# Kernel optimization log

Measured on AMD Instinct MI355X. Metric: run time of the kernel, lower is better.

The kernel has to match this reference:

```python
import jax, jax.numpy as jnp
import numpy as np

K = 5  # neighbors per node


def build_knn_adjacency(x, k=K):
    # x: (B, N, D) -> adj: (B, N, N)
    B, N, D = x.shape
    x_norm = x / jnp.clip(jnp.linalg.norm(x, axis=-1, keepdims=True), 1e-12)
    sim = jnp.einsum('bnd,bmd->bnm', x_norm, x_norm)  # (B, N, N)
    eye = jnp.eye(N, dtype=bool)
    sim = jnp.where(eye[None], jnp.asarray(-1.0, sim.dtype), sim)
    _, knn_idx = jax.lax.top_k(sim, k)  # (B, N, k)
    b_ix = jnp.arange(B)[:, None, None]
    i_ix = jnp.arange(N)[None, :, None]
    adj = jnp.zeros((B, N, N), dtype=x.dtype).at[b_ix, i_ix, knn_idx].set(1.0)
    adj = adj + jnp.eye(N, dtype=x.dtype)[None]
    return adj


def gcn_layer(x, adj, W, b):
    # deg-normalized aggregation then linear (torch Linear: x @ W.T + b)
    deg = adj.sum(axis=-1, keepdims=True)
    adj_norm = adj / jnp.clip(deg, 1.0)
    out = jnp.einsum('bnm,bmd->bnd', adj_norm, x)
    return out @ W.T + b


def setup_inputs() -> dict:
    key = jax.random.key(0)
    k1, k2, k3, k4, k5 = jax.random.split(key, 5)
    B, N, D, H = 32, 1024, 128, 128
    scale = 1.0 / np.sqrt(D)
    return {
        'x': jax.random.normal(k1, (B, N, D), dtype=jnp.float32),
        'W1': jax.random.normal(k2, (H, D), dtype=jnp.float32) * scale,
        'b1': jax.random.normal(k3, (H,), dtype=jnp.float32) * 0.01,
        'W2': jax.random.normal(k4, (H, H), dtype=jnp.float32) * scale,
        'b2': jax.random.normal(k5, (H,), dtype=jnp.float32) * 0.01,
    }


def reference(x, W1, b1, W2, b2):
    adj = build_knn_adjacency(x, k=K)
    h = x + jax.nn.relu(gcn_layer(x, adj, W1, b1))
    h = h + jax.nn.relu(gcn_layer(h, adj, W2, b2))
    return h  # pool='none' -> (B, N, hidden_dim)
```

## Files before the change

kernel.cpp:

```cpp
#include <hip/hip_runtime.h>
#include <float.h>
#include <math.h>

#define BB 32
#define NN 1024
#define DD 128
#define KK 5

typedef __attribute__((ext_vector_type(8))) short bf16x8;
typedef __attribute__((ext_vector_type(4))) float f32x4;

__device__ __forceinline__ unsigned short f2bf(float f) {
    unsigned int u = __float_as_uint(f);
    return (unsigned short)((u + 0x7FFFu + ((u >> 16) & 1u)) >> 16);
}
__device__ __forceinline__ float bf2f(unsigned short h) {
    return __uint_as_float(((unsigned int)h) << 16);
}

__global__ __launch_bounds__(256) void k_norm(const float* __restrict__ x,
                                              unsigned short* __restrict__ ph,
                                              unsigned short* __restrict__ pm,
                                              unsigned short* __restrict__ pl) {
    int row  = blockIdx.x * 4 + (threadIdx.x >> 6);
    int lane = threadIdx.x & 63;
    float2 v = *reinterpret_cast<const float2*>(x + (size_t)row * DD + lane * 2);
    float ss = v.x * v.x + v.y * v.y;
#pragma unroll
    for (int o = 32; o >= 1; o >>= 1) ss += __shfl_xor(ss, o);
    float inv = 1.0f / fmaxf(sqrtf(ss), 1e-12f);
    float y0 = v.x * inv, y1 = v.y * inv;

    unsigned short h0 = f2bf(y0);             float r0 = y0 - bf2f(h0);
    unsigned short m0 = f2bf(r0);             float s0 = r0 - bf2f(m0);
    unsigned short l0 = f2bf(s0);
    unsigned short h1 = f2bf(y1);             float r1 = y1 - bf2f(h1);
    unsigned short m1 = f2bf(r1);             float s1 = r1 - bf2f(m1);
    unsigned short l1 = f2bf(s1);

    size_t o = (size_t)row * DD + lane * 2;
    *reinterpret_cast<unsigned int*>(ph + o) = (unsigned int)h0 | ((unsigned int)h1 << 16);
    *reinterpret_cast<unsigned int*>(pm + o) = (unsigned int)m0 | ((unsigned int)m1 << 16);
    *reinterpret_cast<unsigned int*>(pl + o) = (unsigned int)l0 | ((unsigned int)l1 << 16);
}

__device__ __forceinline__ void stage_plane(const unsigned short* __restrict__ g,
                                            unsigned short (*s)[40], int tid,
                                            size_t rowbase, int c) {
#pragma unroll
    for (int hh = 0; hh < 2; ++hh) {
        int u = tid + (hh << 8);
        int row = u >> 2, q = u & 3;
        const float4 v = *reinterpret_cast<const float4*>(
            g + (rowbase + row) * DD + (c << 5) + (q << 3));
        *reinterpret_cast<float4*>(&s[row][q << 3]) = v;
    }
}

__global__ __launch_bounds__(256, 2) void k_sim(const unsigned short* __restrict__ ph,
                                                const unsigned short* __restrict__ pm,
                                                const unsigned short* __restrict__ pl,
                                                float* __restrict__ sim, int b0) {
    int t  = blockIdx.x;
    int bl = t / 36;
    int p  = t - bl * 36;
    int ti = 0;
    while (p >= 8 - ti) { p -= 8 - ti; ++ti; }
    int tj = ti + p;
    int R  = ti << 7, Cc = tj << 7;

    __shared__ unsigned short Ah[128][40], Am[128][40], Al[128][40];
    __shared__ unsigned short Bh[128][40], Bm[128][40], Bl[128][40];

    int tid  = threadIdx.x;
    int wv   = tid >> 6;
    int lane = tid & 63;
    int wr = (wv >> 1) << 6;
    int wc = (wv & 1) << 6;

    size_t base  = (size_t)(b0 + bl) * NN;
    size_t rbA = base + R, rbB = base + Cc;

    f32x4 acc[4][4];
#pragma unroll
    for (int i = 0; i < 4; ++i)
#pragma unroll
        for (int j = 0; j < 4; ++j) acc[i][j] = (f32x4){0.f, 0.f, 0.f, 0.f};

    int kk = (lane >> 4) << 3;
    int fr = lane & 15;

    for (int c = 0; c < 4; ++c) {
        if (c) __syncthreads();
        stage_plane(ph, Ah, tid, rbA, c);
        stage_plane(pm, Am, tid, rbA, c);
        stage_plane(pl, Al, tid, rbA, c);
        stage_plane(ph, Bh, tid, rbB, c);
        stage_plane(pm, Bm, tid, rbB, c);
        stage_plane(pl, Bl, tid, rbB, c);
        __syncthreads();

        bf16x8 bh[4], bm[4], blo[4];
#pragma unroll
        for (int cp = 0; cp < 4; ++cp) {
            int rb = wc + cp * 16 + fr;
            bh[cp]  = *reinterpret_cast<const bf16x8*>(&Bh[rb][kk]);
            bm[cp]  = *reinterpret_cast<const bf16x8*>(&Bm[rb][kk]);
            blo[cp] = *reinterpret_cast<const bf16x8*>(&Bl[rb][kk]);
        }
#pragma unroll
        for (int rp = 0; rp < 4; ++rp) {
            int ra = wr + rp * 16 + fr;
            bf16x8 ah = *reinterpret_cast<const bf16x8*>(&Ah[ra][kk]);
            bf16x8 am = *reinterpret_cast<const bf16x8*>(&Am[ra][kk]);
            bf16x8 al = *reinterpret_cast<const bf16x8*>(&Al[ra][kk]);
#pragma unroll
            for (int cp = 0; cp < 4; ++cp) {
                f32x4 cacc = acc[rp][cp];
                cacc = __builtin_amdgcn_mfma_f32_16x16x32_bf16(ah, bh[cp],  cacc, 0, 0, 0);
                cacc = __builtin_amdgcn_mfma_f32_16x16x32_bf16(ah, bm[cp],  cacc, 0, 0, 0);
                cacc = __builtin_amdgcn_mfma_f32_16x16x32_bf16(am, bh[cp],  cacc, 0, 0, 0);
                cacc = __builtin_amdgcn_mfma_f32_16x16x32_bf16(ah, blo[cp], cacc, 0, 0, 0);
                cacc = __builtin_amdgcn_mfma_f32_16x16x32_bf16(al, bh[cp],  cacc, 0, 0, 0);
                cacc = __builtin_amdgcn_mfma_f32_16x16x32_bf16(am, bm[cp],  cacc, 0, 0, 0);
                acc[rp][cp] = cacc;
            }
        }
    }

    float* Cb = sim + (size_t)bl * NN * NN;
    int crow = R + wr + ((lane >> 4) << 2);
    int ccol = Cc + wc + fr;
#pragma unroll
    for (int rp = 0; rp < 4; ++rp)
#pragma unroll
        for (int reg = 0; reg < 4; ++reg) {
            size_t rowo = (size_t)(crow + rp * 16 + reg) * NN + ccol;
#pragma unroll
            for (int cp = 0; cp < 4; ++cp)
                Cb[rowo + cp * 16] = acc[rp][cp][reg];
        }
    if (ti != tj) {
#pragma unroll
        for (int cp = 0; cp < 4; ++cp) {
            size_t mr = (size_t)(Cc + wc + cp * 16 + fr) * NN + (R + wr + ((lane >> 4) << 2));
#pragma unroll
            for (int rp = 0; rp < 4; ++rp)
                *reinterpret_cast<float4*>(&Cb[mr + rp * 16]) =
                    make_float4(acc[rp][cp][0], acc[rp][cp][1], acc[rp][cp][2], acc[rp][cp][3]);
        }
    }
}

__global__ __launch_bounds__(256) void k_topk(const float* __restrict__ sim,
                                              int* __restrict__ idx, int b0) {
    int lrow = blockIdx.x * 4 + (threadIdx.x >> 6);
    int lane = threadIdx.x & 63;
    const float* sr = sim + (size_t)lrow * NN;
    int i = lrow & (NN - 1);

    float v[16];
#pragma unroll
    for (int q = 0; q < 4; ++q) {
        float4 f = *reinterpret_cast<const float4*>(sr + lane * 16 + q * 4);
        v[q * 4 + 0] = f.x; v[q * 4 + 1] = f.y; v[q * 4 + 2] = f.z; v[q * 4 + 3] = f.w;
    }
    if ((i >> 4) == lane) {
        int s = i & 15;
#pragma unroll
        for (int j = 0; j < 16; ++j) if (j == s) v[j] = -FLT_MAX;
    }
    int* op = idx + ((size_t)b0 * NN + lrow) * KK;
#pragma unroll
    for (int t = 0; t < KK; ++t) {
        float bv = v[0]; int bj = 0;
#pragma unroll
        for (int j = 1; j < 16; ++j) if (v[j] > bv) { bv = v[j]; bj = j; }
        int bm = (lane << 4) + bj;
#pragma unroll
        for (int o = 1; o < 64; o <<= 1) {
            float ov = __shfl_xor(bv, o);
            int   om = __shfl_xor(bm, o);
            if (ov > bv || (ov == bv && om < bm)) { bv = ov; bm = om; }
        }
        if ((bm >> 4) == lane) {
            int s = bm & 15;
#pragma unroll
            for (int j = 0; j < 16; ++j) if (j == s) v[j] = -FLT_MAX;
        }
        if (lane == 0) op[t] = bm;
    }
}

#define SW(c) ((c) + 4 * ((c) >> 5))
#define LDW 140

__global__ __launch_bounds__(256, 3) void k_gcn(const float* __restrict__ h,
                                                const int* __restrict__ idx,
                                                const float* __restrict__ W,
                                                const float* __restrict__ bias,
                                                const float* __restrict__ res,
                                                float* __restrict__ out) {
    int rt = blockIdx.x << 6;
    __shared__ float As[64][68];
    __shared__ float Bs[64][LDW];
    int tid = threadIdx.x;
    int tr  = (tid >> 4) << 2;
    int tc  = (tid & 15) << 3;
    int stc = SW(tc);

    float acc[4][8];
#pragma unroll
    for (int i = 0; i < 4; ++i)
#pragma unroll
        for (int j = 0; j < 8; ++j) acc[i][j] = 0.f;

#pragma unroll
    for (int kc = 0; kc < 2; ++kc) {
        if (kc) __syncthreads();
        {
            int kv = tid & 15, r0 = tid >> 4;
            int colf = (kc << 6) + (kv << 2);
#pragma unroll
            for (int p = 0; p < 4; ++p) {
                int lrow = r0 + (p << 4);
                int grow = rt + lrow;
                const int* ip = idx + (size_t)grow * KK;
                const float* hb = h + (((size_t)grow >> 10) << 10) * DD;
                float4 v = *reinterpret_cast<const float4*>(h + (size_t)grow * DD + colf);
#pragma unroll
                for (int t = 0; t < KK; ++t) {
                    const float4 u = *reinterpret_cast<const float4*>(hb + (size_t)ip[t] * DD + colf);
                    v.x += u.x; v.y += u.y; v.z += u.z; v.w += u.w;
                }
                const float c = 1.0f / 6.0f;
                int k = kv << 2;
                As[k + 0][lrow] = v.x * c; As[k + 1][lrow] = v.y * c;
                As[k + 2][lrow] = v.z * c; As[k + 3][lrow] = v.w * c;
            }
        }
        {
            int kv = tid & 15, r0 = tid >> 4;
            const float* g = W + kc * 64;
#pragma unroll
            for (int p = 0; p < 8; ++p) {
                int r = r0 + (p << 4);
                const float4 v = *reinterpret_cast<const float4*>(g + (size_t)r * DD + (kv << 2));
                int k = kv << 2, row = SW(r);
                Bs[k + 0][row] = v.x; Bs[k + 1][row] = v.y;
                Bs[k + 2][row] = v.z; Bs[k + 3][row] = v.w;
            }
        }
        __syncthreads();
#pragma unroll 4
        for (int k = 0; k < 64; ++k) {
            const float4 a  = *reinterpret_cast<const float4*>(&As[k][tr]);
            const float4 b0 = *reinterpret_cast<const float4*>(&Bs[k][stc]);
            const float4 b1 = *reinterpret_cast<const float4*>(&Bs[k][stc + 4]);
            const float av[4] = {a.x, a.y, a.z, a.w};
            const float bw[8] = {b0.x, b0.y, b0.z, b0.w, b1.x, b1.y, b1.z, b1.w};
#pragma unroll
            for (int ii = 0; ii < 4; ++ii)
#pragma unroll
                for (int jj = 0; jj < 8; ++jj)
                    acc[ii][jj] = fmaf(av[ii], bw[jj], acc[ii][jj]);
        }
    }
    const float4 bz0 = *reinterpret_cast<const float4*>(bias + tc);
    const float4 bz1 = *reinterpret_cast<const float4*>(bias + tc + 4);
    const float bb[8] = {bz0.x, bz0.y, bz0.z, bz0.w, bz1.x, bz1.y, bz1.z, bz1.w};
#pragma unroll
    for (int i = 0; i < 4; ++i) {
        size_t ro = (size_t)(rt + tr + i) * DD + tc;
        const float4 r0 = *reinterpret_cast<const float4*>(res + ro);
        const float4 r1 = *reinterpret_cast<const float4*>(res + ro + 4);
        float4 o0, o1;
        o0.x = r0.x + fmaxf(acc[i][0] + bb[0], 0.f);
        o0.y = r0.y + fmaxf(acc[i][1] + bb[1], 0.f);
        o0.z = r0.z + fmaxf(acc[i][2] + bb[2], 0.f);
        o0.w = r0.w + fmaxf(acc[i][3] + bb[3], 0.f);
        o1.x = r1.x + fmaxf(acc[i][4] + bb[4], 0.f);
        o1.y = r1.y + fmaxf(acc[i][5] + bb[5], 0.f);
        o1.z = r1.z + fmaxf(acc[i][6] + bb[6], 0.f);
        o1.w = r1.w + fmaxf(acc[i][7] + bb[7], 0.f);
        *reinterpret_cast<float4*>(out + ro)     = o0;
        *reinterpret_cast<float4*>(out + ro + 4) = o1;
    }
}

extern "C" void kernel_launch(void* const* d_in, const int* in_sizes, int n_in,
                              void* d_out, int out_size, void* d_ws, size_t ws_size,
                              hipStream_t stream) {
    const float* x  = (const float*)d_in[0];
    const float* W1 = (const float*)d_in[1];
    const float* b1 = (const float*)d_in[2];
    const float* W2 = (const float*)d_in[3];
    const float* b2 = (const float*)d_in[4];
    float* out = (float*)d_out;

    char* ws = (char*)d_ws;
    size_t pl_b  = (size_t)BB * NN * DD * 2;
    size_t h1_b  = (size_t)BB * NN * DD * 4;
    size_t idx_b = (size_t)BB * NN * KK * 4;
    unsigned short* ph = (unsigned short*)ws;  ws += pl_b;
    unsigned short* pm = (unsigned short*)ws;  ws += pl_b;
    unsigned short* pl = (unsigned short*)ws;  ws += pl_b;
    float* h1  = (float*)ws;                   ws += h1_b;
    int*   idx = (int*)ws;                     ws += idx_b;
    float* sim = (float*)ws;
    size_t fixed = 3 * pl_b + h1_b + idx_b;
    size_t sim_avail = (ws_size > fixed) ? (ws_size - fixed) : 0;
    int SB = (int)(sim_avail / ((size_t)NN * NN * 4));
    if (SB > BB) SB = BB;
    if (SB < 1) SB = 1;

    k_norm<<<BB * NN / 4, 256, 0, stream>>>(x, ph, pm, pl);
    for (int b0 = 0; b0 < BB; b0 += SB) {
        int sb = (SB < BB - b0) ? SB : (BB - b0);
        k_sim<<<sb * 36, 256, 0, stream>>>(ph, pm, pl, sim, b0);
        k_topk<<<sb * NN / 4, 256, 0, stream>>>(sim, idx, b0);
    }
    k_gcn<<<BB * NN / 64, 256, 0, stream>>>(x,  idx, W1, b1, x,  h1);
    k_gcn<<<BB * NN / 64, 256, 0, stream>>>(h1, idx, W2, b2, h1, out);
}
```

Measured before the change: 172.1 us.

## Fuse top-k selection into similarity GEMM epilogue with partial candidate merge

Instead of writing the full N×N similarity matrix to global memory and running a separate top-k pass, each sim tile now computes per-row top-5 candidates in registers and shared memory, then writes them to a compact candidate buffer. A new merge kernel reduces the 16 partial candidate lists per row into the final 5 indices. This removes the large sim write and read traffic and the per-batch launch loop, at the cost of extra selection work in the GEMM epilogue. The block index is also swizzled across batches.

```diff
diff --git a/kernel.cpp b/kernel.cpp
--- a/kernel.cpp
+++ b/kernel.cpp
@@ -9,6 +9,7 @@
 
 typedef __attribute__((ext_vector_type(8))) short bf16x8;
 typedef __attribute__((ext_vector_type(4))) float f32x4;
+typedef unsigned long long ull;
 
 __device__ __forceinline__ unsigned short f2bf(float f) {
     unsigned int u = __float_as_uint(f);
@@ -16,6 +17,21 @@
 }
 __device__ __forceinline__ float bf2f(unsigned short h) {
     return __uint_as_float(((unsigned int)h) << 16);
+}
+
+__device__ __forceinline__ ull mkkey(float v, int col) {
+    unsigned int u = __float_as_uint(v);
+    unsigned int ou = u ^ (unsigned)((((int)u) >> 31) | 0x80000000);
+    return ((ull)ou << 32) | (unsigned)(1023 - col);
+}
+
+__device__ __forceinline__ void ins5(ull k, ull* s) {
+    bool b0 = k > s[0], b1 = k > s[1], b2 = k > s[2], b3 = k > s[3], b4 = k > s[4];
+    s[4] = b4 ? (b3 ? s[3] : k) : s[4];
+    s[3] = b3 ? (b2 ? s[2] : k) : s[3];
+    s[2] = b2 ? (b1 ? s[1] : k) : s[2];
+    s[1] = b1 ? (b0 ? s[0] : k) : s[1];
+    s[0] = b0 ? k : s[0];
 }
 
 __global__ __launch_bounds__(256) void k_norm(const float* __restrict__ x,
@@ -44,41 +60,50 @@
     *reinterpret_cast<unsigned int*>(pl + o) = (unsigned int)l0 | ((unsigned int)l1 << 16);
 }
 
+union SMem {
+    struct {
+        unsigned short Ah[128][40], Am[128][40], Al[128][40];
+        unsigned short Bh[128][40], Bm[128][40], Bl[128][40];
+    } s;
+    float q[4][32][68];
+};
+
 __device__ __forceinline__ void stage_plane(const unsigned short* __restrict__ g,
                                             unsigned short (*s)[40], int tid,
                                             size_t rowbase, int c) {
 #pragma unroll
     for (int hh = 0; hh < 2; ++hh) {
         int u = tid + (hh << 8);
-        int row = u >> 2, q = u & 3;
+        int row = u >> 2, qq = u & 3;
         const float4 v = *reinterpret_cast<const float4*>(
-            g + (rowbase + row) * DD + (c << 5) + (q << 3));
-        *reinterpret_cast<float4*>(&s[row][q << 3]) = v;
+            g + (rowbase + row) * DD + (c << 5) + (qq << 3));
+        *reinterpret_cast<float4*>(&s[row][qq << 3]) = v;
     }
 }
 
 __global__ __launch_bounds__(256, 2) void k_sim(const unsigned short* __restrict__ ph,
                                                 const unsigned short* __restrict__ pm,
                                                 const unsigned short* __restrict__ pl,
-                                                float* __restrict__ sim, int b0) {
-    int t  = blockIdx.x;
-    int bl = t / 36;
-    int p  = t - bl * 36;
+                                                ull* __restrict__ cand) {
+    int bid = blockIdx.x;
+    int lb  = (bid & 7) * 144 + (bid >> 3);
+    int bl  = lb / 36;
+    int p   = lb - bl * 36;
     int ti = 0;
     while (p >= 8 - ti) { p -= 8 - ti; ++ti; }
     int tj = ti + p;
     int R  = ti << 7, Cc = tj << 7;
 
-    __shared__ unsigned short Ah[128][40], Am[128][40], Al[128][40];
-    __shared__ unsigned short Bh[128][40], Bm[128][40], Bl[128][40];
+    __shared__ SMem sm;
 
     int tid  = threadIdx.x;
     int wv   = tid >> 6;
     int lane = tid & 63;
     int wr = (wv >> 1) << 6;
     int wc = (wv & 1) << 6;
-
-    size_t base  = (size_t)(b0 + bl) * NN;
+    int lg = lane >> 4, fr = lane & 15;
+
+    size_t base = (size_t)bl * NN;
     size_t rbA = base + R, rbB = base + Cc;
 
     f32x4 acc[4][4];
@@ -87,33 +112,32 @@
 #pragma unroll
         for (int j = 0; j < 4; ++j) acc[i][j] = (f32x4){0.f, 0.f, 0.f, 0.f};
 
-    int kk = (lane >> 4) << 3;
-    int fr = lane & 15;
+    int kk = lg << 3;
 
     for (int c = 0; c < 4; ++c) {
         if (c) __syncthreads();
-        stage_plane(ph, Ah, tid, rbA, c);
-        stage_plane(pm, Am, tid, rbA, c);
-        stage_plane(pl, Al, tid, rbA, c);
-        stage_plane(ph, Bh, tid, rbB, c);
-        stage_plane(pm, Bm, tid, rbB, c);
-        stage_plane(pl, Bl, tid, rbB, c);
+        stage_plane(ph, sm.s.Ah, tid, rbA, c);
+        stage_plane(pm, sm.s.Am, tid, rbA, c);
+        stage_plane(pl, sm.s.Al, tid, rbA, c);
+        stage_plane(ph, sm.s.Bh, tid, rbB, c);
+        stage_plane(pm, sm.s.Bm, tid, rbB, c);
+        stage_plane(pl, sm.s.Bl, tid, rbB, c);
         __syncthreads();
 
         bf16x8 bh[4], bm[4], blo[4];
 #pragma unroll
         for (int cp = 0; cp < 4; ++cp) {
             int rb = wc + cp * 16 + fr;
-            bh[cp]  = *reinterpret_cast<const bf16x8*>(&Bh[rb][kk]);
-            bm[cp]  = *reinterpret_cast<const bf16x8*>(&Bm[rb][kk]);
-            blo[cp] = *reinterpret_cast<const bf16x8*>(&Bl[rb][kk]);
+            bh[cp]  = *reinterpret_cast<const bf16x8*>(&sm.s.Bh[rb][kk]);
+            bm[cp]  = *reinterpret_cast<const bf16x8*>(&sm.s.Bm[rb][kk]);
+            blo[cp] = *reinterpret_cast<const bf16x8*>(&sm.s.Bl[rb][kk]);
         }
 #pragma unroll
         for (int rp = 0; rp < 4; ++rp) {
             int ra = wr + rp * 16 + fr;
-            bf16x8 ah = *reinterpret_cast<const bf16x8*>(&Ah[ra][kk]);
-            bf16x8 am = *reinterpret_cast<const bf16x8*>(&Am[ra][kk]);
-            bf16x8 al = *reinterpret_cast<const bf16x8*>(&Al[ra][kk]);
+            bf16x8 ah = *reinterpret_cast<const bf16x8*>(&sm.s.Ah[ra][kk]);
+            bf16x8 am = *reinterpret_cast<const bf16x8*>(&sm.s.Am[ra][kk]);
+            bf16x8 al = *reinterpret_cast<const bf16x8*>(&sm.s.Al[ra][kk]);
 #pragma unroll
             for (int cp = 0; cp < 4; ++cp) {
                 f32x4 cacc = acc[rp][cp];
@@ -128,67 +152,82 @@
         }
     }
 
-    float* Cb = sim + (size_t)bl * NN * NN;
-    int crow = R + wr + ((lane >> 4) << 2);
-    int ccol = Cc + wc + fr;
-#pragma unroll
-    for (int rp = 0; rp < 4; ++rp)
-#pragma unroll
-        for (int reg = 0; reg < 4; ++reg) {
-            size_t rowo = (size_t)(crow + rp * 16 + reg) * NN + ccol;
-#pragma unroll
-            for (int cp = 0; cp < 4; ++cp)
-                Cb[rowo + cp * 16] = acc[rp][cp][reg];
-        }
+    __syncthreads();
+
+    ull s5[5] = {0, 0, 0, 0, 0};
+    int grow = R + wr + lane;
+#pragma unroll
+    for (int hp = 0; hp < 2; ++hp) {
+#pragma unroll
+        for (int rp = 0; rp < 4; ++rp)
+#pragma unroll
+            for (int cpl = 0; cpl < 2; ++cpl) {
+                int cp = 2 * hp + cpl;
+                *reinterpret_cast<float4*>(&sm.q[wv][cpl * 16 + fr][rp * 16 + lg * 4]) =
+                    *reinterpret_cast<float4*>(&acc[rp][cp]);
+            }
+#pragma unroll
+        for (int c = 0; c < 32; ++c) {
+            float v = sm.q[wv][c][lane];
+            int gc = Cc + wc + 32 * hp + c;
+            ull key = mkkey(v, gc);
+            if (gc == grow) key = 0;
+            ins5(key, s5);
+        }
+    }
+    {
+        int slot = 2 * tj + (wc >> 6);
+        ull* o = cand + ((base + grow) * 16 + slot) * 5;
+        o[0] = s5[0]; o[1] = s5[1]; o[2] = s5[2]; o[3] = s5[3]; o[4] = s5[4];
+    }
+
     if (ti != tj) {
+        int slot = 2 * ti + (wr >> 6);
 #pragma unroll
         for (int cp = 0; cp < 4; ++cp) {
-            size_t mr = (size_t)(Cc + wc + cp * 16 + fr) * NN + (R + wr + ((lane >> 4) << 2));
+            ull m5[5] = {0, 0, 0, 0, 0};
 #pragma unroll
             for (int rp = 0; rp < 4; ++rp)
-                *reinterpret_cast<float4*>(&Cb[mr + rp * 16]) =
-                    make_float4(acc[rp][cp][0], acc[rp][cp][1], acc[rp][cp][2], acc[rp][cp][3]);
-        }
-    }
-}
-
-__global__ __launch_bounds__(256) void k_topk(const float* __restrict__ sim,
-                                              int* __restrict__ idx, int b0) {
-    int lrow = blockIdx.x * 4 + (threadIdx.x >> 6);
-    int lane = threadIdx.x & 63;
-    const float* sr = sim + (size_t)lrow * NN;
-    int i = lrow & (NN - 1);
-
-    float v[16];
-#pragma unroll
-    for (int q = 0; q < 4; ++q) {
-        float4 f = *reinterpret_cast<const float4*>(sr + lane * 16 + q * 4);
-        v[q * 4 + 0] = f.x; v[q * 4 + 1] = f.y; v[q * 4 + 2] = f.z; v[q * 4 + 3] = f.w;
-    }
-    if ((i >> 4) == lane) {
-        int s = i & 15;
-#pragma unroll
-        for (int j = 0; j < 16; ++j) if (j == s) v[j] = -FLT_MAX;
-    }
-    int* op = idx + ((size_t)b0 * NN + lrow) * KK;
-#pragma unroll
-    for (int t = 0; t < KK; ++t) {
-        float bv = v[0]; int bj = 0;
-#pragma unroll
-        for (int j = 1; j < 16; ++j) if (v[j] > bv) { bv = v[j]; bj = j; }
-        int bm = (lane << 4) + bj;
-#pragma unroll
-        for (int o = 1; o < 64; o <<= 1) {
-            float ov = __shfl_xor(bv, o);
-            int   om = __shfl_xor(bm, o);
-            if (ov > bv || (ov == bv && om < bm)) { bv = ov; bm = om; }
-        }
-        if ((bm >> 4) == lane) {
-            int s = bm & 15;
-#pragma unroll
-            for (int j = 0; j < 16; ++j) if (j == s) v[j] = -FLT_MAX;
-        }
-        if (lane == 0) op[t] = bm;
+#pragma unroll
+                for (int rg = 0; rg < 4; ++rg) {
+                    int gr2 = R + wr + rp * 16 + lg * 4 + rg;
+                    ins5(mkkey(acc[rp][cp][rg], gr2), m5);
+                }
+            int mnode = Cc + wc + cp * 16 + fr;
+            ull* o = cand + ((base + mnode) * 16 + slot) * 5;
+            ull k0 = m5[0], k1 = m5[1], k2 = m5[2], k3 = m5[3], k4 = m5[4];
+#pragma unroll
+            for (int t = 0; t < 5; ++t) {
+                ull w = k0;
+                ull x = __shfl_xor(w, 16); if (x > w) w = x;
+                x     = __shfl_xor(w, 32); if (x > w) w = x;
+                if (lg == 0) o[t] = w;
+                bool adv = (k0 == w);
+                k0 = adv ? k1 : k0; k1 = adv ? k2 : k1;
+                k2 = adv ? k3 : k2; k3 = adv ? k4 : k3; k4 = adv ? 0ULL : k4;
+            }
+        }
+    }
+}
+
+__global__ __launch_bounds__(256) void k_merge(const ull* __restrict__ cand,
+                                               int* __restrict__ idx) {
+    int row = blockIdx.x * 16 + (threadIdx.x >> 4);
+    int g   = threadIdx.x & 15;
+    const ull* cp = cand + ((size_t)row * 16 + g) * 5;
+    ull k0 = cp[0], k1 = cp[1], k2 = cp[2], k3 = cp[3], k4 = cp[4];
+    int* op = idx + (size_t)row * KK;
+#pragma unroll
+    for (int t = 0; t < 5; ++t) {
+        ull w = k0;
+#pragma unroll
+        for (int o = 1; o < 16; o <<= 1) {
+            ull x = __shfl_xor(w, o); if (x > w) w = x;
+        }
+        if (g == t) op[t] = 1023 - (int)(w & 0xFFFFFFFFu);
+        bool adv = (k0 == w);
+        k0 = adv ? k1 : k0; k1 = adv ? k2 : k1;
+        k2 = adv ? k3 : k2; k3 = adv ? k4 : k3; k4 = adv ? 0ULL : k4;
     }
 }
 
@@ -222,8 +261,8 @@
             int kv = tid & 15, r0 = tid >> 4;
             int colf = (kc << 6) + (kv << 2);
 #pragma unroll
-            for (int p = 0; p < 4; ++p) {
-                int lrow = r0 + (p << 4);
+            for (int pq = 0; pq < 4; ++pq) {
+                int lrow = r0 + (pq << 4);
                 int grow = rt + lrow;
                 const int* ip = idx + (size_t)grow * KK;
                 const float* hb = h + (((size_t)grow >> 10) << 10) * DD;
@@ -243,8 +282,8 @@
             int kv = tid & 15, r0 = tid >> 4;
             const float* g = W + kc * 64;
 #pragma unroll
-            for (int p = 0; p < 8; ++p) {
-                int r = r0 + (p << 4);
+            for (int pq = 0; pq < 8; ++pq) {
+                int r = r0 + (pq << 4);
                 const float4 v = *reinterpret_cast<const float4*>(g + (size_t)r * DD + (kv << 2));
                 int k = kv << 2, row = SW(r);
                 Bs[k + 0][row] = v.x; Bs[k + 1][row] = v.y;
@@ -299,27 +338,20 @@
     float* out = (float*)d_out;
 
     char* ws = (char*)d_ws;
-    size_t pl_b  = (size_t)BB * NN * DD * 2;
-    size_t h1_b  = (size_t)BB * NN * DD * 4;
-    size_t idx_b = (size_t)BB * NN * KK * 4;
+    size_t pl_b   = (size_t)BB * NN * DD * 2;
+    size_t h1_b   = (size_t)BB * NN * DD * 4;
+    size_t idx_b  = (size_t)BB * NN * KK * 4;
+    size_t cand_b = (size_t)BB * NN * 16 * 5 * 8;
     unsigned short* ph = (unsigned short*)ws;  ws += pl_b;
     unsigned short* pm = (unsigned short*)ws;  ws += pl_b;
     unsigned short* pl = (unsigned short*)ws;  ws += pl_b;
     float* h1  = (float*)ws;                   ws += h1_b;
     int*   idx = (int*)ws;                     ws += idx_b;
-    float* sim = (float*)ws;
-    size_t fixed = 3 * pl_b + h1_b + idx_b;
-    size_t sim_avail = (ws_size > fixed) ? (ws_size - fixed) : 0;
-    int SB = (int)(sim_avail / ((size_t)NN * NN * 4));
-    if (SB > BB) SB = BB;
-    if (SB < 1) SB = 1;
+    ull*  cand = (ull*)ws;                     ws += cand_b;
 
     k_norm<<<BB * NN / 4, 256, 0, stream>>>(x, ph, pm, pl);
-    for (int b0 = 0; b0 < BB; b0 += SB) {
-        int sb = (SB < BB - b0) ? SB : (BB - b0);
-        k_sim<<<sb * 36, 256, 0, stream>>>(ph, pm, pl, sim, b0);
-        k_topk<<<sb * NN / 4, 256, 0, stream>>>(sim, idx, b0);
-    }
+    k_sim<<<BB * 36, 256, 0, stream>>>(ph, pm, pl, cand);
+    k_merge<<<BB * NN / 16, 256, 0, stream>>>(cand, idx);
     k_gcn<<<BB * NN / 64, 256, 0, stream>>>(x,  idx, W1, b1, x,  h1);
     k_gcn<<<BB * NN / 64, 256, 0, stream>>>(h1, idx, W2, b2, h1, out);
 }
```

New measurement: 255.7 us. 48.6% more time.
